# Kernel tuning notes

Hardware: AMD Instinct MI355X
Metric: run time of the kernel (lower is better)

## Reference

```python
import jax, jax.numpy as jnp
import numpy as np

SUP = 7
EPS = 1e-12

def _gather(t, idx):
    # t: (b, v, d), idx: (b, v, n) -> (b, v, n, d)
    return jax.vmap(lambda tb, ib: tb[ib])(t, idx)

def _knn(v, k):
    # squared pairwise distance, exclude self (smallest), return k neighbors
    q = jnp.sum(v * v, axis=-1)
    d = q[:, :, None] + q[:, None, :] - 2.0 * jnp.einsum('bid,bjd->bij', v, v)
    _, idx = jax.lax.top_k(-d, k + 1)
    return idx[:, :, 1:]

def _dir_norm(v, idx):
    d = _gather(v, idx) - v[:, :, None, :]
    n = jnp.sqrt(jnp.sum(d * d, axis=-1, keepdims=True))
    return d / jnp.maximum(n, EPS)

def _col_norm(d):
    n = jnp.sqrt(jnp.sum(d * d, axis=0, keepdims=True))
    return d / jnp.maximum(n, EPS)

def _conv_surface(idx, v, directions, kernel_num):
    theta = jax.nn.silu(_dir_norm(v, idx) @ _col_norm(directions))  # (b,V,n,SUP*K)
    b, V, n, _ = theta.shape
    theta = theta.reshape(b, V, n, SUP, kernel_num)
    return jnp.sum(jnp.max(theta, axis=2), axis=2)

def _conv_layer(idx, v, fm, W, bias, directions, out_c):
    b, V, n = idx.shape
    theta = jax.nn.silu(_dir_norm(v, idx) @ _col_norm(directions))  # (b,V,n,SUP*out_c)
    feat = fm @ W + bias                                             # (b,V,(SUP+1)*out_c)
    center = feat[:, :, :out_c]
    support = _gather(feat[:, :, out_c:], idx)                       # (b,V,n,SUP*out_c)
    act = (theta * support).reshape(b, V, n, SUP, out_c)
    act = jnp.sum(jnp.max(act, axis=2), axis=2)
    return center + act

def _bn(x, g, b, eps=1e-5):
    # BatchNorm1d in training mode: stats over batch and vertex dims
    m = jnp.mean(x, axis=(0, 1))
    var = jnp.var(x, axis=(0, 1))
    return (x - m) / jnp.sqrt(var + eps) * g + b

def _nearest(target, source):
    d = (jnp.sum(source * source, -1)[:, None, :] + jnp.sum(target * target, -1)[:, :, None]
         - 2.0 * jnp.einsum('bid,bjd->bij', target, source))
    return jnp.argmin(d, axis=-1)  # (b, v1)

def _forward(x, d0, w1, b1, dir1, g1, bb1, w2, b2, dir2, g2, bb2,
             w3, b3, dir3, g3, bb3, w4, b4, dir4, perm1, perm2):
    nb = _knn(x, 10)
    fm0 = jax.nn.silu(_conv_surface(nb, x, d0, 128))
    fm1 = jax.nn.silu(_bn(_conv_layer(nb, x, fm0, w1, b1, dir1, 128), g1, bb1))
    # pool 1: max over 4-NN features, then subsample to V/4
    pooled = jnp.max(_gather(fm1, _knn(x, 4)), axis=2)
    v1 = x[:, perm1]
    f1 = pooled[:, perm1]
    nb = _knn(v1, 10)
    fm2 = jax.nn.silu(_bn(_conv_layer(nb, v1, f1, w2, b2, dir2, 256), g2, bb2))
    fm3 = jax.nn.silu(_bn(_conv_layer(nb, v1, fm2, w3, b3, dir3, 256), g3, bb3))
    # pool 2
    pooled = jnp.max(_gather(fm3, _knn(v1, 4)), axis=2)
    v2 = v1[:, perm2]
    f2 = pooled[:, perm2]
    nb = _knn(v2, 10)
    fm4 = _conv_layer(nb, v2, f2, w4, b4, dir4, 512)
    n1 = _nearest(x, v1)
    n2 = _nearest(x, v2)
    up = lambda f, i: jax.vmap(lambda fb, ib: fb[ib])(f, i)
    return jnp.concatenate([fm0, fm1, up(fm2, n1), up(fm3, n1), up(fm4, n2)], axis=-1)

def setup_inputs() -> dict:
    key = jax.random.key(0)
    ks = jax.random.split(key, 24)
    B, V = 2, 4096
    uni = lambda k, shape, s: jax.random.uniform(k, shape, jnp.float32, -s, s)
    s1 = (128 * (SUP + 1)) ** -0.5
    s2 = (256 * (SUP + 1)) ** -0.5
    s4 = (512 * (SUP + 1)) ** -0.5
    s0 = (SUP * 128) ** -0.5
    inp = {
        'x': jax.random.normal(ks[0], (B, V, 3), jnp.float32),
        'd0': uni(ks[1], (3, SUP * 128), s0),
        'w1': uni(ks[2], (128, (SUP + 1) * 128), s1),
        'b1': uni(ks[3], ((SUP + 1) * 128,), s1),
        'dir1': uni(ks[4], (3, SUP * 128), s1),
        'g1': jnp.ones((128,), jnp.float32),
        'bb1': jnp.zeros((128,), jnp.float32),
        'w2': uni(ks[5], (128, (SUP + 1) * 256), s2),
        'b2': uni(ks[6], ((SUP + 1) * 256,), s2),
        'dir2': uni(ks[7], (3, SUP * 256), s2),
        'g2': jnp.ones((256,), jnp.float32),
        'bb2': jnp.zeros((256,), jnp.float32),
        'w3': uni(ks[8], (256, (SUP + 1) * 256), s2),
        'b3': uni(ks[9], ((SUP + 1) * 256,), s2),
        'dir3': uni(ks[10], (3, SUP * 256), s2),
        'g3': jnp.ones((256,), jnp.float32),
        'bb3': jnp.zeros((256,), jnp.float32),
        'w4': uni(ks[11], (256, (SUP + 1) * 512), s4),
        'b4': uni(ks[12], ((SUP + 1) * 512,), s4),
        'dir4': uni(ks[13], (3, SUP * 512), s4),
        'perm1': jax.random.permutation(ks[20], V)[: V // 4].astype(jnp.int32),
        'perm2': jax.random.permutation(ks[21], V // 4)[: V // 16].astype(jnp.int32),
    }
    return inp

def reference(x, d0, w1, b1, dir1, g1, bb1, w2, b2, dir2, g2, bb2,
              w3, b3, dir3, g3, bb3, w4, b4, dir4, perm1, perm2):
    return _forward(x, d0, w1, b1, dir1, g1, bb1, w2, b2, dir2, g2, bb2,
                    w3, b3, dir3, g3, bb3, w4, b4, dir4, perm1, perm2)
```

## Files before the change

kernel.cpp:

```cpp
#include <hip/hip_runtime.h>
#include <math.h>
#include <float.h>
#include <limits.h>

#define BNUM 2
#define V0 4096
#define V1N 1024
#define V2N 256
#define SUPN 7

typedef float float4v __attribute__((ext_vector_type(4)));
typedef float float2v __attribute__((ext_vector_type(2)));
typedef unsigned short ushort4v __attribute__((ext_vector_type(4)));
typedef unsigned long long u64;

__device__ __forceinline__ float fast_silu(float x){
  return __fdividef(x, 1.0f + __expf(-x));
}

__device__ __forceinline__ unsigned short f2bf(float f){
  unsigned int u=__float_as_uint(f);
  u += 0x7FFFu + ((u>>16)&1u);
  return (unsigned short)(u>>16);
}
__device__ __forceinline__ float bf2f(unsigned short h){
  return __uint_as_float(((unsigned int)h)<<16);
}

__device__ __forceinline__ unsigned int fkey(float f){
  unsigned int u = __float_as_uint(f);
  int m = ((int)u) >> 31;
  return u ^ (unsigned int)(m | 0x80000000);
}

__device__ __forceinline__ u64 shfl_xor_u64(u64 v, int m){
  unsigned int lo = (unsigned int)v, hi = (unsigned int)(v>>32);
  lo = (unsigned int)__shfl_xor((int)lo, m);
  hi = (unsigned int)__shfl_xor((int)hi, m);
  return ((u64)hi<<32) | lo;
}

__global__ void colnorm_all_k(const float* __restrict__ d0, const float* __restrict__ dir1,
                              const float* __restrict__ dir2, const float* __restrict__ dir3,
                              const float* __restrict__ dir4,
                              float* __restrict__ cn0, float* __restrict__ cn1,
                              float* __restrict__ cn2, float* __restrict__ cn3,
                              float* __restrict__ cn4, float* __restrict__ stats){
  int c = blockIdx.x*256 + threadIdx.x;
  if(c < 1280) stats[c] = 0.0f;
  const float* s; float* o; int nc;
  if(c < 896){ s=d0; o=cn0; nc=896; }
  else if((c-=896) < 896){ s=dir1; o=cn1; nc=896; }
  else if((c-=896) < 1792){ s=dir2; o=cn2; nc=1792; }
  else if((c-=1792) < 1792){ s=dir3; o=cn3; nc=1792; }
  else { c-=1792; if(c>=3584) return; s=dir4; o=cn4; nc=3584; }
  float a=s[c], b=s[nc+c], e=s[2*nc+c];
  float n=sqrtf(a*a+b*b+e*e); n=fmaxf(n,1e-12f);
  o[c]=a/n; o[nc+c]=b/n; o[2*nc+c]=e/n;
}

template<int VC, int THREADS, int MINW>
__global__ __launch_bounds__(THREADS, MINW) void knn10_k(const float* __restrict__ pts,
    int* __restrict__ out_idx, float* __restrict__ out_dirn)
{
  constexpr int CHUNK = VC/64;
  constexpr int QPB = THREADS/64;
  __shared__ float4v sp4[VC];
  __shared__ float sdd[QPB][34];
  __shared__ int   sdi[QPB][34];
  int t = threadIdx.x;
  int lane = t & 63;
  int wv   = t >> 6;
  int b = blockIdx.y;
  int j = blockIdx.x*QPB + wv;
  const float* pb = pts + (size_t)b*VC*3;
  for(int i=t; i<VC; i+=THREADS){
    float x=pb[3*i], y=pb[3*i+1], z=pb[3*i+2];
    float4v v; v[0]=x; v[1]=y; v[2]=z; v[3]=x*x+y*y+z*z;
    sp4[i]=v;
  }
  __syncthreads();
  float qx=pb[3*j], qy=pb[3*j+1], qz=pb[3*j+2];
  float qs=qx*qx+qy*qy+qz*qz;

  float dc[CHUNK];
  float p0=INFINITY, p1=INFINITY, p2=INFINITY, p3=INFINITY;
  #pragma unroll
  for(int c=0;c<CHUNK;c++){
    float4v p = sp4[c*64+lane];
    float dot = qx*p[0]+qy*p[1]+qz*p[2];
    float d = fmaf(-2.0f, dot, p[3]+qs);
    dc[c]=d;
    float s=d, a;
    a=fminf(p0,s); s=fmaxf(p0,s); p0=a;
    a=fminf(p1,s); s=fmaxf(p1,s); p1=a;
    a=fminf(p2,s); s=fmaxf(p2,s); p2=a;
    p3=fminf(p3,s);
  }

  float prev=-INFINITY;
  for(int sel=0; sel<11; ++sel){
    float cand = p0>prev ? p0 : (p1>prev ? p1 : (p2>prev ? p2 : (p3>prev ? p3 : INFINITY)));
    #pragma unroll
    for(int s=32;s;s>>=1) cand = fminf(cand, __shfl_xor(cand, s));
    prev=cand;
  }
  float v11 = prev;

  int cnt=0;
  #pragma unroll
  for(int c=0;c<CHUNK;c++){
    bool hit = dc[c] <= v11;
    u64 m = __ballot(hit);
    if(m){
      if(hit){
        int pos = cnt + __popcll(m & ((1ull<<lane)-1ull));
        if(pos<32){ sdd[wv][pos]=dc[c]; sdi[wv][pos]=c*64+lane; }
      }
      cnt += (int)__popcll(m);
    }
  }
  if(cnt>32) cnt=32;

  if(lane < cnt){
    float dl = sdd[wv][lane]; int il = sdi[wv][lane];
    int rank=0;
    for(int m2=0;m2<cnt;m2++){
      float dm=sdd[wv][m2]; int im=sdi[wv][m2];
      rank += (dm<dl || (dm==dl && im<il)) ? 1 : 0;
    }
    if(rank>=1 && rank<=10){
      size_t obase=((size_t)b*VC+j)*10 + (rank-1);
      out_idx[obase]=il;
      float4v p = sp4[il];
      float dx=p[0]-qx, dy=p[1]-qy, dz=p[2]-qz;
      float n=sqrtf(dx*dx+dy*dy+dz*dz); n=fmaxf(n,1e-12f);
      out_dirn[obase*3]=dx/n; out_dirn[obase*3+1]=dy/n; out_dirn[obase*3+2]=dz/n;
    }
  }
}

template<int NODES>
__global__ __launch_bounds__(64*NODES) void conv_surf_k(
    const float* __restrict__ dirn, const float* __restrict__ cnd,
    float* __restrict__ fm0, float* __restrict__ outbuf)
{
  int tid=threadIdx.x, nd=tid>>6, t=tid&63;
  int b=blockIdx.y, i=blockIdx.x*NODES+nd;
  __shared__ float sd[NODES][32];
  if(t<30) sd[nd][t]=dirn[((size_t)(b*V0+i))*30+t];
  __syncthreads();
  float acc0=0.0f, acc1=0.0f;
  for(int s=0;s<SUPN;s++){
    int col=s*128+t;
    float wa0=cnd[col],     wa1=cnd[896+col],     wa2=cnd[1792+col];
    float wb0=cnd[col+64],  wb1=cnd[896+col+64],  wb2=cnd[1792+col+64];
    float m0=-INFINITY, m1=-INFINITY;
    #pragma unroll
    for(int n=0;n<10;n++){
      float dx=sd[nd][3*n], dy=sd[nd][3*n+1], dz=sd[nd][3*n+2];
      m0=fmaxf(m0, fast_silu(dx*wa0+dy*wa1+dz*wa2));
      m1=fmaxf(m1, fast_silu(dx*wb0+dy*wb1+dz*wb2));
    }
    acc0+=m0; acc1+=m1;
  }
  float r0=fast_silu(acc0), r1=fast_silu(acc1);
  size_t frow=(size_t)(b*V0+i)*128;
  fm0[frow+t]=r0; fm0[frow+64+t]=r1;
  size_t orow=(size_t)(b*V0+i)*1280;
  outbuf[orow+t]=r0; outbuf[orow+64+t]=r1;
}

__global__ __launch_bounds__(256) void gemm_split_k(
    const float* __restrict__ A, const float* __restrict__ W,
    const float* __restrict__ bias,
    float* __restrict__ Cc, unsigned short* __restrict__ Sp,
    int M, int N, int K, int outC)
{
  __shared__ float As[16][132];
  __shared__ float Bs[16][132];
  int t=threadIdx.x;
  int tx=t&15, ty=t>>4;
  int bm=blockIdx.y*128, bn=blockIdx.x*128;
  float4v acc[2][2][4];
  #pragma unroll
  for(int a=0;a<2;a++)
    #pragma unroll
    for(int bidx=0;bidx<2;bidx++)
      #pragma unroll
      for(int m=0;m<4;m++) acc[a][bidx][m]=(float4v)(0.0f);
  int arow=t>>2, akk=(t&3)*4;
  int brow=t>>4, bcol=(t&15)*4;
  const float* Aa=&A[(size_t)(bm+arow)*K    + akk];
  const float* Ab=&A[(size_t)(bm+64+arow)*K + akk];
  const float* Wa=&W[(size_t)brow*N + bn+bcol];
  const float* Wb=&W[(size_t)brow*N + bn+64+bcol];
  float4v a0=*(const float4v*)Aa;
  float4v a1=*(const float4v*)Ab;
  float4v b0=*(const float4v*)Wa;
  float4v b1=*(const float4v*)Wb;
  for(int k0=0;k0<K;k0+=16){
    __syncthreads();
    #pragma unroll
    for(int u=0;u<4;u++){ As[akk+u][arow]=a0[u]; As[akk+u][64+arow]=a1[u]; }
    *(float4v*)&Bs[brow][bcol]=b0;
    *(float4v*)&Bs[brow][64+bcol]=b1;
    __syncthreads();
    if(k0+16<K){
      a0=*(const float4v*)(Aa + k0+16);
      a1=*(const float4v*)(Ab + k0+16);
      b0=*(const float4v*)(Wa + (size_t)(k0+16)*N);
      b1=*(const float4v*)(Wb + (size_t)(k0+16)*N);
    }
    #pragma unroll
    for(int kk=0;kk<16;kk++){
      float4v alo=*(const float4v*)&As[kk][ty*4];
      float4v ahi=*(const float4v*)&As[kk][64+ty*4];
      float4v blo=*(const float4v*)&Bs[kk][tx*4];
      float4v bhi=*(const float4v*)&Bs[kk][64+tx*4];
      #pragma unroll
      for(int mi=0;mi<4;mi++){
        acc[0][0][mi] += alo[mi]*blo;
        acc[0][1][mi] += alo[mi]*bhi;
        acc[1][0][mi] += ahi[mi]*blo;
        acc[1][1][mi] += ahi[mi]*bhi;
      }
    }
  }
  float4v bl=*(const float4v*)&bias[bn+tx*4];
  float4v bh=*(const float4v*)&bias[bn+64+tx*4];
  if(bn + 128 <= outC){
    #pragma unroll
    for(int mh=0;mh<2;mh++)
      #pragma unroll
      for(int mi=0;mi<4;mi++){
        size_t row=(size_t)(bm+mh*64+ty*4+mi);
        *(float4v*)&Cc[row*outC + bn+tx*4]    = acc[mh][0][mi]+bl;
        *(float4v*)&Cc[row*outC + bn+64+tx*4] = acc[mh][1][mi]+bh;
      }
  } else {
    int sw = 7*outC;
    int scol = bn - outC;
    #pragma unroll
    for(int mh=0;mh<2;mh++)
      #pragma unroll
      for(int mi=0;mi<4;mi++){
        size_t row=(size_t)(bm+mh*64+ty*4+mi);
        float4v r0=acc[mh][0][mi]+bl, r1=acc[mh][1][mi]+bh;
        ushort4v p0,p1;
        #pragma unroll
        for(int u=0;u<4;u++){ p0[u]=f2bf(r0[u]); p1[u]=f2bf(r1[u]); }
        *(ushort4v*)&Sp[row*sw + scol+tx*4]    = p0;
        *(ushort4v*)&Sp[row*sw + scol+64+tx*4] = p1;
      }
  }
}

template<int C, int TPN, int NODES>
__global__ __launch_bounds__(TPN*NODES) void conv_agg_k(
    const float* __restrict__ cent, const unsigned short* __restrict__ sup,
    int Vb,
    const float* __restrict__ dirn, const int* __restrict__ nbidx,
    const float* __restrict__ cnd,
    float* __restrict__ outp, float* __restrict__ stats)
{
  constexpr int ncol = SUPN*C;
  constexpr int NT = TPN*NODES;
  int tid=threadIdx.x, nd=tid/TPN, t=tid%TPN;
  int b=blockIdx.y, i=blockIdx.x*NODES+nd;
  __shared__ float sd[NODES][32];
  __shared__ int snb[NODES][12];
  __shared__ float ssum[C], ssq[C];
  __shared__ float scn[3*ncol];
  if(t<30) sd[nd][t]=dirn[((size_t)(b*Vb+i))*30+t];
  if(t<10) snb[nd][t]=nbidx[(size_t)(b*Vb+i)*10+t];
  for(int c=tid;c<3*ncol;c+=NT) scn[c]=cnd[c];
  if(stats) for(int c=tid;c<C;c+=NT){ ssum[c]=0.0f; ssq[c]=0.0f; }
  __syncthreads();

  const int col0 = t*4;
  const unsigned short* fb = sup + (size_t)b*Vb*ncol;

  float m[SUPN][4];
  #pragma unroll
  for(int s=0;s<SUPN;s++)
    #pragma unroll
    for(int v=0;v<4;v++) m[s][v]=-INFINITY;

  ushort4v bufA[SUPN], bufB[SUPN];
  float dax,day,daz, dbx,dby,dbz;
  {
    unsigned int off=(unsigned int)snb[nd][0]*ncol + col0;
    #pragma unroll
    for(int s=0;s<SUPN;s++) bufA[s]=*(const ushort4v*)&fb[off + s*C];
    dax=sd[nd][0]; day=sd[nd][1]; daz=sd[nd][2];
  }
  #pragma unroll 1
  for(int np=0;np<5;np++){
    {
      int nn=2*np+1;
      unsigned int off=(unsigned int)snb[nd][nn]*ncol + col0;
      #pragma unroll
      for(int s=0;s<SUPN;s++) bufB[s]=*(const ushort4v*)&fb[off + s*C];
      dbx=sd[nd][3*nn]; dby=sd[nd][3*nn+1]; dbz=sd[nd][3*nn+2];
    }
    #pragma unroll
    for(int s=0;s<SUPN;s++){
      int cb=s*C+col0;
      float4v w0=*(const float4v*)&scn[cb];
      float4v w1=*(const float4v*)&scn[ncol+cb];
      float4v w2=*(const float4v*)&scn[2*ncol+cb];
      ushort4v sv=bufA[s];
      #pragma unroll
      for(int v=0;v<4;v++){
        float d = dax*w0[v] + day*w1[v] + daz*w2[v];
        m[s][v] = fmaxf(m[s][v], fast_silu(d)*bf2f(sv[v]));
      }
    }
    if(np<4){
      int nn=2*np+2;
      unsigned int off=(unsigned int)snb[nd][nn]*ncol + col0;
      #pragma unroll
      for(int s=0;s<SUPN;s++) bufA[s]=*(const ushort4v*)&fb[off + s*C];
      dax=sd[nd][3*nn]; day=sd[nd][3*nn+1]; daz=sd[nd][3*nn+2];
    }
    #pragma unroll
    for(int s=0;s<SUPN;s++){
      int cb=s*C+col0;
      float4v w0=*(const float4v*)&scn[cb];
      float4v w1=*(const float4v*)&scn[ncol+cb];
      float4v w2=*(const float4v*)&scn[2*ncol+cb];
      ushort4v sv=bufB[s];
      #pragma unroll
      for(int v=0;v<4;v++){
        float d = dbx*w0[v] + dby*w1[v] + dbz*w2[v];
        m[s][v] = fmaxf(m[s][v], fast_silu(d)*bf2f(sv[v]));
      }
    }
  }

  float acc[4];
  {
    float4v cv=*(const float4v*)&cent[(size_t)(b*Vb+i)*C + col0];
    #pragma unroll
    for(int v=0;v<4;v++){
      acc[v]=cv[v];
      #pragma unroll
      for(int s=0;s<SUPN;s++) acc[v]+=m[s][v];
    }
  }
  {
    float4v ov;
    #pragma unroll
    for(int v=0;v<4;v++) ov[v]=acc[v];
    *(float4v*)&outp[(size_t)(b*Vb+i)*C + col0]=ov;
  }
  if(stats){
    #pragma unroll
    for(int v=0;v<4;v++){
      atomicAdd(&ssum[col0+v], acc[v]);
      atomicAdd(&ssq[col0+v], acc[v]*acc[v]);
    }
    __syncthreads();
    for(int c=tid;c<C;c+=NT){
      atomicAdd(&stats[c], ssum[c]);
      atomicAdd(&stats[C+c], ssq[c]);
    }
  }
}

__global__ void bn_silu_k(const float* __restrict__ xin, const float* __restrict__ sums,
                          float invM, int C, const float* __restrict__ g, const float* __restrict__ bb,
                          float* __restrict__ y, int nquad, float* __restrict__ osl, int cshift)
{
  int gid=blockIdx.x*blockDim.x+threadIdx.x;
  if(gid>=nquad) return;
  int base=gid*4;
  int c=base&(C-1);
  float4v xv=*(const float4v*)&xin[base];
  float4v sm=*(const float4v*)&sums[c];
  float4v sq=*(const float4v*)&sums[C+c];
  float4v gv=*(const float4v*)&g[c];
  float4v bv=*(const float4v*)&bb[c];
  float4v r;
  #pragma unroll
  for(int u=0;u<4;u++){
    float mean=sm[u]*invM;
    float var=sq[u]*invM - mean*mean;
    float v=(xv[u]-mean)*rsqrtf(var+1e-5f)*gv[u]+bv[u];
    r[u]=fast_silu(v);
  }
  *(float4v*)&y[base]=r;
  if(osl){
    int row=base>>cshift;
    *(float4v*)&osl[(size_t)row*1280 + c]=r;
  }
}

template<int C, int NODES>
__global__ __launch_bounds__((C/4)*NODES) void pool_gather_k(
    const float* __restrict__ fm, int Vsrc,
    const int* __restrict__ idx10, const int* __restrict__ perm,
    const float* __restrict__ vsrc,
    float* __restrict__ fout, float* __restrict__ vout, int Vq)
{
  constexpr int TPN=C/4;
  int tid=threadIdx.x, nd=tid/TPN, t=tid%TPN;
  int b=blockIdx.y, j=blockIdx.x*NODES+nd;
  int r=perm[j];
  const int* id=idx10+((size_t)b*Vsrc+r)*10;
  const float* fb=fm+(size_t)b*Vsrc*C;
  float4v m=(float4v)(-INFINITY);
  #pragma unroll
  for(int n=0;n<4;n++){
    float4v fv=*(const float4v*)&fb[(size_t)id[n]*C + t*4];
    #pragma unroll
    for(int u=0;u<4;u++) m[u]=fmaxf(m[u],fv[u]);
  }
  *(float4v*)&fout[(size_t)(b*Vq+j)*C + t*4]=m;
  if(t<3) vout[((size_t)b*Vq+j)*3+t]=vsrc[((size_t)b*Vsrc+r)*3+t];
}

__global__ __launch_bounds__(512) void nearest_concat_k(
    const float* __restrict__ v1, const float* __restrict__ v2,
    const float* __restrict__ x,
    const float* __restrict__ fm2, const float* __restrict__ fm3,
    const float* __restrict__ fm4,
    float* __restrict__ outp)
{
  __shared__ float4v s1[V1N];
  __shared__ float4v s2[V2N];
  int t=threadIdx.x;
  int lane=t&63, wv=t>>6;
  int b=blockIdx.y; int j=blockIdx.x*8+wv;
  const float* c1=v1+(size_t)b*V1N*3;
  const float* c2=v2+(size_t)b*V2N*3;
  for(int i=t;i<V1N;i+=512){
    float xx=c1[3*i],yy=c1[3*i+1],zz=c1[3*i+2];
    float4v v; v[0]=xx;v[1]=yy;v[2]=zz;v[3]=xx*xx+yy*yy+zz*zz; s1[i]=v;
  }
  for(int i=t;i<V2N;i+=512){
    float xx=c2[3*i],yy=c2[3*i+1],zz=c2[3*i+2];
    float4v v; v[0]=xx;v[1]=yy;v[2]=zz;v[3]=xx*xx+yy*yy+zz*zz; s2[i]=v;
  }
  __syncthreads();
  const float* qb=x+(size_t)b*V0*3;
  float qx=qb[3*j],qy=qb[3*j+1],qz=qb[3*j+2];
  float qs=qx*qx+qy*qy+qz*qz;
  u64 bk=~0ull;
  #pragma unroll 4
  for(int c=0;c<V1N/64;c++){
    int i=c*64+lane;
    float4v p=s1[i];
    float dot=qx*p[0]+qy*p[1]+qz*p[2];
    float d=fmaf(-2.0f,dot,p[3]+qs);
    u64 k=((u64)fkey(d)<<32)|(unsigned int)i;
    bk = k<bk ? k : bk;
  }
  #pragma unroll
  for(int s=32;s;s>>=1){ u64 o=shfl_xor_u64(bk,s); bk = o<bk?o:bk; }
  int j1=(int)(bk&0xffffffffu);
  bk=~0ull;
  #pragma unroll 4
  for(int c=0;c<V2N/64;c++){
    int i=c*64+lane;
    float4v p=s2[i];
    float dot=qx*p[0]+qy*p[1]+qz*p[2];
    float d=fmaf(-2.0f,dot,p[3]+qs);
    u64 k=((u64)fkey(d)<<32)|(unsigned int)i;
    bk = k<bk ? k : bk;
  }
  #pragma unroll
  for(int s=32;s;s>>=1){ u64 o=shfl_xor_u64(bk,s); bk = o<bk?o:bk; }
  int j2=(int)(bk&0xffffffffu);

  const float4v* f2p=(const float4v*)(fm2 + ((size_t)b*V1N+j1)*256);
  const float4v* f3p=(const float4v*)(fm3 + ((size_t)b*V1N+j1)*256);
  const float4v* f4p=(const float4v*)(fm4 + ((size_t)b*V2N+j2)*512);
  float4v* op=(float4v*)(outp + (size_t)(b*V0+j)*1280) + 64;
  op[lane]       = f2p[lane];
  op[64+lane]    = f3p[lane];
  op[128+lane]   = f4p[lane];
  op[192+lane]   = f4p[64+lane];
}

extern "C" void kernel_launch(void* const* d_in, const int* in_sizes, int n_in,
                              void* d_out, int out_size, void* d_ws, size_t ws_size,
                              hipStream_t stream) {
  const float* x   =(const float*)d_in[0];
  const float* d0  =(const float*)d_in[1];
  const float* w1  =(const float*)d_in[2];
  const float* b1  =(const float*)d_in[3];
  const float* dir1=(const float*)d_in[4];
  const float* g1  =(const float*)d_in[5];
  const float* bb1 =(const float*)d_in[6];
  const float* w2  =(const float*)d_in[7];
  const float* b2  =(const float*)d_in[8];
  const float* dir2=(const float*)d_in[9];
  const float* g2  =(const float*)d_in[10];
  const float* bb2 =(const float*)d_in[11];
  const float* w3  =(const float*)d_in[12];
  const float* b3  =(const float*)d_in[13];
  const float* dir3=(const float*)d_in[14];
  const float* g3  =(const float*)d_in[15];
  const float* bb3 =(const float*)d_in[16];
  const float* w4  =(const float*)d_in[17];
  const float* b4  =(const float*)d_in[18];
  const float* dir4=(const float*)d_in[19];
  const int* perm1 =(const int*)d_in[20];
  const int* perm2 =(const int*)d_in[21];
  float* out=(float*)d_out;

  float* w=(float*)d_ws;
  size_t off=0;
  auto alloc=[&](size_t n){ float* p=w+off; off+=n; return p; };
  float* cn0 =alloc(2688);
  float* cn1 =alloc(2688);
  float* cn2 =alloc(5376);
  float* cn3 =alloc(5376);
  float* cn4 =alloc(10752);
  float* dirnx =alloc((size_t)BNUM*V0*30);
  float* dirnv1=alloc((size_t)BNUM*V1N*30);
  float* dirnv2=alloc((size_t)BNUM*V2N*30);
  float* fm0 =alloc((size_t)BNUM*V0*128);
  float* cent=alloc((size_t)BNUM*V0*128);
  unsigned short* supb=(unsigned short*)alloc((size_t)BNUM*V0*896/2);
  float* fm1r=alloc((size_t)BNUM*V0*128);
  float* fm1 =alloc((size_t)BNUM*V0*128);
  float* f1  =alloc((size_t)BNUM*V1N*128);
  float* v1  =alloc((size_t)BNUM*V1N*3);
  float* fm2r=alloc((size_t)BNUM*V1N*256);
  float* fm2 =alloc((size_t)BNUM*V1N*256);
  float* fm3r=alloc((size_t)BNUM*V1N*256);
  float* fm3 =alloc((size_t)BNUM*V1N*256);
  float* f2  =alloc((size_t)BNUM*V2N*256);
  float* v2  =alloc((size_t)BNUM*V2N*3);
  float* fm4 =alloc((size_t)BNUM*V2N*512);
  float* stats=alloc(1280);
  int* idx10x =(int*)alloc((size_t)BNUM*V0*10);
  int* idx10v1=(int*)alloc((size_t)BNUM*V1N*10);
  int* idx10v2=(int*)alloc((size_t)BNUM*V2N*10);

  colnorm_all_k<<<dim3(35),256,0,stream>>>(d0,dir1,dir2,dir3,dir4,cn0,cn1,cn2,cn3,cn4,stats);

  knn10_k<V0,1024,4><<<dim3(V0/16,BNUM),1024,0,stream>>>(x, idx10x, dirnx);
  conv_surf_k<4><<<dim3(V0/4,BNUM),256,0,stream>>>(dirnx, cn0, fm0, out);

  gemm_split_k<<<dim3(1024/128,(BNUM*V0)/128),256,0,stream>>>(fm0, w1, b1, cent, supb, BNUM*V0, 1024, 128, 128);
  conv_agg_k<128,32,8><<<dim3(V0/8,BNUM),256,0,stream>>>(cent, supb, V0, dirnx, idx10x, cn1, fm1r, stats);
  bn_silu_k<<<dim3((BNUM*V0*128/4)/256),256,0,stream>>>(fm1r, stats, 1.0f/(BNUM*V0), 128, g1, bb1, fm1, BNUM*V0*128/4, out+128, 7);

  pool_gather_k<128,8><<<dim3(V1N/8,BNUM),256,0,stream>>>(fm1, V0, idx10x, perm1, x, f1, v1, V1N);

  knn10_k<V1N,256,6><<<dim3(V1N/4,BNUM),256,0,stream>>>(v1, idx10v1, dirnv1);

  gemm_split_k<<<dim3(2048/128,(BNUM*V1N)/128),256,0,stream>>>(f1, w2, b2, cent, supb, BNUM*V1N, 2048, 128, 256);
  conv_agg_k<256,64,4><<<dim3(V1N/4,BNUM),256,0,stream>>>(cent, supb, V1N, dirnv1, idx10v1, cn2, fm2r, stats+256);
  bn_silu_k<<<dim3((BNUM*V1N*256/4)/256),256,0,stream>>>(fm2r, stats+256, 1.0f/(BNUM*V1N), 256, g2, bb2, fm2, BNUM*V1N*256/4, nullptr, 8);

  gemm_split_k<<<dim3(2048/128,(BNUM*V1N)/128),256,0,stream>>>(fm2, w3, b3, cent, supb, BNUM*V1N, 2048, 256, 256);
  conv_agg_k<256,64,4><<<dim3(V1N/4,BNUM),256,0,stream>>>(cent, supb, V1N, dirnv1, idx10v1, cn3, fm3r, stats+768);
  bn_silu_k<<<dim3((BNUM*V1N*256/4)/256),256,0,stream>>>(fm3r, stats+768, 1.0f/(BNUM*V1N), 256, g3, bb3, fm3, BNUM*V1N*256/4, nullptr, 8);

  pool_gather_k<256,4><<<dim3(V2N/4,BNUM),256,0,stream>>>(fm3, V1N, idx10v1, perm2, v1, f2, v2, V2N);

  knn10_k<V2N,256,6><<<dim3(V2N/4,BNUM),256,0,stream>>>(v2, idx10v2, dirnv2);

  gemm_split_k<<<dim3(4096/128,(BNUM*V2N)/128),256,0,stream>>>(f2, w4, b4, cent, supb, BNUM*V2N, 4096, 256, 512);
  conv_agg_k<512,128,2><<<dim3(V2N/2,BNUM),256,0,stream>>>(cent, supb, V2N, dirnv2, idx10v2, cn4, fm4, nullptr);

  nearest_concat_k<<<dim3(V0/8,BNUM),512,0,stream>>>(v1, v2, x, fm2, fm3, fm4, out);
}
```

Before: 480.7 us.

## Replace FP32 SIMT GEMM with split-bf16 MFMA GEMM emulating fp32 precision

```diff
diff --git a/kernel.cpp b/kernel.cpp
--- a/kernel.cpp
+++ b/kernel.cpp
@@ -12,6 +12,9 @@
 typedef float float4v __attribute__((ext_vector_type(4)));
 typedef float float2v __attribute__((ext_vector_type(2)));
 typedef unsigned short ushort4v __attribute__((ext_vector_type(4)));
+typedef unsigned short ushort8v __attribute__((ext_vector_type(8)));
+typedef short short8v __attribute__((ext_vector_type(8)));
+typedef __bf16 bf16x8 __attribute__((ext_vector_type(8)));
 typedef unsigned long long u64;
 
 __device__ __forceinline__ float fast_silu(float x){
@@ -171,88 +174,128 @@
   outbuf[orow+t]=r0; outbuf[orow+64+t]=r1;
 }
 
-__global__ __launch_bounds__(256) void gemm_split_k(
+__global__ __launch_bounds__(256) void gemm_mfma_k(
     const float* __restrict__ A, const float* __restrict__ W,
     const float* __restrict__ bias,
     float* __restrict__ Cc, unsigned short* __restrict__ Sp,
     int M, int N, int K, int outC)
 {
-  __shared__ float As[16][132];
-  __shared__ float Bs[16][132];
+  __shared__ __attribute__((aligned(16))) unsigned short Ah[128][48];
+  __shared__ __attribute__((aligned(16))) unsigned short Al[128][48];
+  __shared__ __attribute__((aligned(16))) unsigned short Bh[128][48];
+  __shared__ __attribute__((aligned(16))) unsigned short Bl[128][48];
   int t=threadIdx.x;
-  int tx=t&15, ty=t>>4;
+  int lane=t&63, wv=t>>6;
+  int wr=(wv>>1)*64, wc=(wv&1)*64;
   int bm=blockIdx.y*128, bn=blockIdx.x*128;
-  float4v acc[2][2][4];
-  #pragma unroll
-  for(int a=0;a<2;a++)
-    #pragma unroll
-    for(int bidx=0;bidx<2;bidx++)
-      #pragma unroll
-      for(int m=0;m<4;m++) acc[a][bidx][m]=(float4v)(0.0f);
-  int arow=t>>2, akk=(t&3)*4;
-  int brow=t>>4, bcol=(t&15)*4;
-  const float* Aa=&A[(size_t)(bm+arow)*K    + akk];
-  const float* Ab=&A[(size_t)(bm+64+arow)*K + akk];
-  const float* Wa=&W[(size_t)brow*N + bn+bcol];
-  const float* Wb=&W[(size_t)brow*N + bn+64+bcol];
-  float4v a0=*(const float4v*)Aa;
-  float4v a1=*(const float4v*)Ab;
-  float4v b0=*(const float4v*)Wa;
-  float4v b1=*(const float4v*)Wb;
-  for(int k0=0;k0<K;k0+=16){
+
+  float4v acc[4][4];
+  #pragma unroll
+  for(int fi=0;fi<4;fi++)
+    #pragma unroll
+    for(int fj=0;fj<4;fj++) acc[fi][fj]=(float4v)(0.0f);
+
+  int ar=t>>1, af=(t&1)*4;
+  const float* Ag = A + (size_t)(bm+ar)*K + af*4;
+  int nn=t&127, kb0=t>>7;
+  const float* Wg = W + bn + nn;
+
+  float4v pa[4];
+  float pb[2][8];
+  #pragma unroll
+  for(int q=0;q<4;q++) pa[q]=*(const float4v*)(Ag + q*4);
+  #pragma unroll
+  for(int j=0;j<8;j++){
+    pb[0][j]=Wg[(size_t)(kb0*8+j)*N];
+    pb[1][j]=Wg[(size_t)((kb0+2)*8+j)*N];
+  }
+
+  for(int k0=0;k0<K;k0+=32){
     __syncthreads();
     #pragma unroll
-    for(int u=0;u<4;u++){ As[akk+u][arow]=a0[u]; As[akk+u][64+arow]=a1[u]; }
-    *(float4v*)&Bs[brow][bcol]=b0;
-    *(float4v*)&Bs[brow][64+bcol]=b1;
+    for(int q=0;q<4;q++){
+      ushort4v hv, lv;
+      #pragma unroll
+      for(int i2=0;i2<4;i2++){
+        float x=pa[q][i2];
+        unsigned short h=f2bf(x);
+        hv[i2]=h;
+        lv[i2]=f2bf(x - bf2f(h));
+      }
+      *(ushort4v*)&Ah[ar][(af+q)*4]=hv;
+      *(ushort4v*)&Al[ar][(af+q)*4]=lv;
+    }
+    #pragma unroll
+    for(int task=0;task<2;task++){
+      int kb=kb0+task*2;
+      ushort8v hv, lv;
+      #pragma unroll
+      for(int j=0;j<8;j++){
+        float x=pb[task][j];
+        unsigned short h=f2bf(x);
+        hv[j]=h;
+        lv[j]=f2bf(x - bf2f(h));
+      }
+      *(ushort8v*)&Bh[nn][kb*8]=hv;
+      *(ushort8v*)&Bl[nn][kb*8]=lv;
+    }
     __syncthreads();
-    if(k0+16<K){
-      a0=*(const float4v*)(Aa + k0+16);
-      a1=*(const float4v*)(Ab + k0+16);
-      b0=*(const float4v*)(Wa + (size_t)(k0+16)*N);
-      b1=*(const float4v*)(Wb + (size_t)(k0+16)*N);
-    }
-    #pragma unroll
-    for(int kk=0;kk<16;kk++){
-      float4v alo=*(const float4v*)&As[kk][ty*4];
-      float4v ahi=*(const float4v*)&As[kk][64+ty*4];
-      float4v blo=*(const float4v*)&Bs[kk][tx*4];
-      float4v bhi=*(const float4v*)&Bs[kk][64+tx*4];
-      #pragma unroll
-      for(int mi=0;mi<4;mi++){
-        acc[0][0][mi] += alo[mi]*blo;
-        acc[0][1][mi] += alo[mi]*bhi;
-        acc[1][0][mi] += ahi[mi]*blo;
-        acc[1][1][mi] += ahi[mi]*bhi;
+    if(k0+32<K){
+      #pragma unroll
+      for(int q=0;q<4;q++) pa[q]=*(const float4v*)(Ag + k0+32 + q*4);
+      #pragma unroll
+      for(int j=0;j<8;j++){
+        pb[0][j]=Wg[(size_t)(k0+32+kb0*8+j)*N];
+        pb[1][j]=Wg[(size_t)(k0+32+(kb0+2)*8+j)*N];
       }
     }
-  }
-  float4v bl=*(const float4v*)&bias[bn+tx*4];
-  float4v bh=*(const float4v*)&bias[bn+64+tx*4];
-  if(bn + 128 <= outC){
-    #pragma unroll
-    for(int mh=0;mh<2;mh++)
-      #pragma unroll
-      for(int mi=0;mi<4;mi++){
-        size_t row=(size_t)(bm+mh*64+ty*4+mi);
-        *(float4v*)&Cc[row*outC + bn+tx*4]    = acc[mh][0][mi]+bl;
-        *(float4v*)&Cc[row*outC + bn+64+tx*4] = acc[mh][1][mi]+bh;
+    int fr=lane&15;
+    int koff=(lane>>4)*8;
+    union { short8v s; bf16x8 b; } Bfh[4], Bfl[4];
+    #pragma unroll
+    for(int fj=0;fj<4;fj++){
+      Bfh[fj].s = *(const short8v*)&Bh[wc+fj*16+fr][koff];
+      Bfl[fj].s = *(const short8v*)&Bl[wc+fj*16+fr][koff];
+    }
+    #pragma unroll
+    for(int fi=0;fi<4;fi++){
+      union { short8v s; bf16x8 b; } Afh, Afl;
+      Afh.s = *(const short8v*)&Ah[wr+fi*16+fr][koff];
+      Afl.s = *(const short8v*)&Al[wr+fi*16+fr][koff];
+      #pragma unroll
+      for(int fj=0;fj<4;fj++){
+        acc[fi][fj] = __builtin_amdgcn_mfma_f32_16x16x32_bf16(Afh.b, Bfh[fj].b, acc[fi][fj], 0,0,0);
+        acc[fi][fj] = __builtin_amdgcn_mfma_f32_16x16x32_bf16(Afh.b, Bfl[fj].b, acc[fi][fj], 0,0,0);
+        acc[fi][fj] = __builtin_amdgcn_mfma_f32_16x16x32_bf16(Afl.b, Bfh[fj].b, acc[fi][fj], 0,0,0);
       }
+    }
+  }
+
+  int fr=lane&15, r0=(lane>>4)*4;
+  float bb4[4];
+  #pragma unroll
+  for(int fj=0;fj<4;fj++) bb4[fj]=bias[bn+wc+fj*16+fr];
+  if(bn+128<=outC){
+    #pragma unroll
+    for(int fi=0;fi<4;fi++)
+      #pragma unroll
+      for(int fj=0;fj<4;fj++)
+        #pragma unroll
+        for(int rg=0;rg<4;rg++){
+          size_t row=(size_t)(bm+wr+fi*16+r0+rg);
+          Cc[row*outC + bn+wc+fj*16+fr]=acc[fi][fj][rg]+bb4[fj];
+        }
   } else {
-    int sw = 7*outC;
-    int scol = bn - outC;
-    #pragma unroll
-    for(int mh=0;mh<2;mh++)
-      #pragma unroll
-      for(int mi=0;mi<4;mi++){
-        size_t row=(size_t)(bm+mh*64+ty*4+mi);
-        float4v r0=acc[mh][0][mi]+bl, r1=acc[mh][1][mi]+bh;
-        ushort4v p0,p1;
+    int sw=7*outC, scol=bn-outC;
+    #pragma unroll
+    for(int fi=0;fi<4;fi++)
+      #pragma unroll
+      for(int fj=0;fj<4;fj++)
         #pragma unroll
-        for(int u=0;u<4;u++){ p0[u]=f2bf(r0[u]); p1[u]=f2bf(r1[u]); }
-        *(ushort4v*)&Sp[row*sw + scol+tx*4]    = p0;
-        *(ushort4v*)&Sp[row*sw + scol+64+tx*4] = p1;
-      }
+        for(int rg=0;rg<4;rg++){
+          size_t row=(size_t)(bm+wr+fi*16+r0+rg);
+          Sp[row*sw + scol+wc+fj*16+fr]=f2bf(acc[fi][fj][rg]+bb4[fj]);
+        }
   }
 }
 
@@ -546,7 +589,7 @@
   knn10_k<V0,1024,4><<<dim3(V0/16,BNUM),1024,0,stream>>>(x, idx10x, dirnx);
   conv_surf_k<4><<<dim3(V0/4,BNUM),256,0,stream>>>(dirnx, cn0, fm0, out);
 
-  gemm_split_k<<<dim3(1024/128,(BNUM*V0)/128),256,0,stream>>>(fm0, w1, b1, cent, supb, BNUM*V0, 1024, 128, 128);
+  gemm_mfma_k<<<dim3(1024/128,(BNUM*V0)/128),256,0,stream>>>(fm0, w1, b1, cent, supb, BNUM*V0, 1024, 128, 128);
   conv_agg_k<128,32,8><<<dim3(V0/8,BNUM),256,0,stream>>>(cent, supb, V0, dirnx, idx10x, cn1, fm1r, stats);
   bn_silu_k<<<dim3((BNUM*V0*128/4)/256),256,0,stream>>>(fm1r, stats, 1.0f/(BNUM*V0), 128, g1, bb1, fm1, BNUM*V0*128/4, out+128, 7);
 
@@ -554,11 +597,11 @@
 
   knn10_k<V1N,256,6><<<dim3(V1N/4,BNUM),256,0,stream>>>(v1, idx10v1, dirnv1);
 
-  gemm_split_k<<<dim3(2048/128,(BNUM*V1N)/128),256,0,stream>>>(f1, w2, b2, cent, supb, BNUM*V1N, 2048, 128, 256);
+  gemm_mfma_k<<<dim3(2048/128,(BNUM*V1N)/128),256,0,stream>>>(f1, w2, b2, cent, supb, BNUM*V1N, 2048, 128, 256);
   conv_agg_k<256,64,4><<<dim3(V1N/4,BNUM),256,0,stream>>>(cent, supb, V1N, dirnv1, idx10v1, cn2, fm2r, stats+256);
   bn_silu_k<<<dim3((BNUM*V1N*256/4)/256),256,0,stream>>>(fm2r, stats+256, 1.0f/(BNUM*V1N), 256, g2, bb2, fm2, BNUM*V1N*256/4, nullptr, 8);
 
-  gemm_split_k<<<dim3(2048/128,(BNUM*V1N)/128),256,0,stream>>>(fm2, w3, b3, cent, supb, BNUM*V1N, 2048, 256, 256);
+  gemm_mfma_k<<<dim3(2048/128,(BNUM*V1N)/128),256,0,stream>>>(fm2, w3, b3, cent, supb, BNUM*V1N, 2048, 256, 256);
   conv_agg_k<256,64,4><<<dim3(V1N/4,BNUM),256,0,stream>>>(cent, supb, V1N, dirnv1, idx10v1, cn3, fm3r, stats+768);
   bn_silu_k<<<dim3((BNUM*V1N*256/4)/256),256,0,stream>>>(fm3r, stats+768, 1.0f/(BNUM*V1N), 256, g3, bb3, fm3, BNUM*V1N*256/4, nullptr, 8);
 
@@ -566,7 +609,7 @@
 
   knn10_k<V2N,256,6><<<dim3(V2N/4,BNUM),256,0,stream>>>(v2, idx10v2, dirnv2);
 
-  gemm_split_k<<<dim3(4096/128,(BNUM*V2N)/128),256,0,stream>>>(f2, w4, b4, cent, supb, BNUM*V2N, 4096, 256, 512);
+  gemm_mfma_k<<<dim3(4096/128,(BNUM*V2N)/128),256,0,stream>>>(f2, w4, b4, cent, supb, BNUM*V2N, 4096, 256, 512);
   conv_agg_k<512,128,2><<<dim3(V2N/2,BNUM),256,0,stream>>>(cent, supb, V2N, dirnv2, idx10v2, cn4, fm4, nullptr);
 
   nearest_concat_k<<<dim3(V0/8,BNUM),512,0,stream>>>(v1, v2, x, fm2, fm3, fm4, out);
```

Result: faster. 442.7 us, median of 2 (-7.9%).
